# Kernel optimization log

Hardware: AMD Instinct MI355X
Metric: run time of the kernel (lower is better)

## Reference

```python
import jax, jax.numpy as jnp
import numpy as np

# Concrete segmented-polynomial instance (uniform 1d):
N = 8192      # nodes (rows of input 0 and of the indexed output)
E = 16384     # edges (batch dim of input 1 and of the per-edge product)
S = 16        # segments per operand (buffer_num_segments, same for all 3 operands)
EXT = 64      # operand_extent (uniform segment shape)
P = 2048      # num_paths of the single operation


def setup_inputs() -> dict:
    key = jax.random.key(0)
    k0, k1, k2, k3, k4, k5 = jax.random.split(key, 6)
    x = jax.random.normal(k0, (N, S * EXT), dtype=jnp.float32)          # node features
    y = jax.random.normal(k1, (E, S * EXT), dtype=jnp.float32)          # edge features
    idx_in = jax.random.randint(k2, (E,), 0, N, dtype=jnp.int32)        # gather index for input 0
    idx_out = jax.random.randint(k3, (E,), 0, N, dtype=jnp.int32)       # scatter index for output 0
    path_indices = jax.random.randint(k4, (P, 3), 0, S, dtype=jnp.int32)  # (i_x, j_y, k_out) per path
    path_coefficients = jax.random.normal(k5, (P,), dtype=jnp.float32)
    return {
        "x": x, "y": y,
        "idx_in": idx_in, "idx_out": idx_out,
        "path_indices": path_indices,
        "path_coefficients": path_coefficients,
    }


def reference(x, y, idx_in, idx_out, path_indices, path_coefficients):
    # Dense path-coefficient tensor C[k, i, j]: duplicate paths accumulate,
    # missing (k,i,j) triples are zero. This is the math-dtype (fp32) contraction
    # the uniform-1d kernel performs over segments of equal extent.
    C = jnp.zeros((S, S, S), dtype=x.dtype).at[
        path_indices[:, 2], path_indices[:, 0], path_indices[:, 1]
    ].add(path_coefficients)

    xr = x.reshape(N, S, EXT)[idx_in]   # gather (BATCH_DIM_INDEXED input): [E, S, EXT]
    yr = y.reshape(E, S, EXT)           # batched input:                    [E, S, EXT]

    # out_e[e, k, c] = sum_{i,j} C[k,i,j] * xr[e,i,c] * yr[e,j,c]
    out_e = jnp.einsum('kij,eic,ejc->ekc', C, xr, yr)

    # scatter-add (BATCH_DIM_INDEXED output) into N output rows
    out = jnp.zeros((N, S, EXT), dtype=x.dtype).at[idx_out].add(out_e)
    return out.reshape(N, S * EXT)
```

## Files before the change

### kernel.cpp

```cpp
#include <hip/hip_runtime.h>
#include <hip/hip_bf16.h>

#define N_NODES 8192
#define E_EDGES 16384
#define S_SEG   16
#define EXT     64
#define P_PATHS 2048
#define ROW     1024
#define L_SLOTS 8
#define NWAVES  (E_EDGES / L_SLOTS)
#define NBLK    (NWAVES / 4)

typedef _Float16 f16x8  __attribute__((ext_vector_type(8)));
typedef _Float16 f16x4  __attribute__((ext_vector_type(4)));
typedef _Float16 half2v __attribute__((ext_vector_type(2)));
typedef float    f32x4  __attribute__((ext_vector_type(4)));

#define WS_CMAT  0
#define WS_HIST  8192
#define WS_CURS  40960
#define WS_ROWS  73728
#define WS_ELIST 106512
#define WS_XRS   172048
#define WS_NDS   237584

__global__ void prep(const int* __restrict__ pidx, const float* __restrict__ pcoef,
                     _Float16* __restrict__ Cmat, int* __restrict__ hist) {
    const int tid = threadIdx.x;
    if (blockIdx.x < 32) { hist[blockIdx.x * 256 + tid] = 0; return; }
    __shared__ float sC[S_SEG * S_SEG * S_SEG];
    for (int i = tid; i < 4096; i += 256) sC[i] = 0.f;
    __syncthreads();
    for (int p = tid; p < P_PATHS; p += 256) {
        int i = pidx[3 * p + 0];
        int j = pidx[3 * p + 1];
        int k = pidx[3 * p + 2];
        atomicAdd(&sC[(k * S_SEG + i) * S_SEG + j], pcoef[p]);
    }
    __syncthreads();
    for (int i = tid; i < 4096; i += 256) Cmat[i] = (_Float16)sC[i];
}

__global__ void hist_k(const int* __restrict__ idx_out, int* __restrict__ hist) {
    const int e = blockIdx.x * 256 + threadIdx.x;
    atomicAdd(&hist[idx_out[e]], 1);
}

__global__ __launch_bounds__(256) void scan_k(const int* __restrict__ hist,
                                              int* __restrict__ rows,
                                              int* __restrict__ cursor) {
    __shared__ int part[256];
    const int t = threadIdx.x;
    const int base = t * 32;
    int loc[32];
    int s = 0;
#pragma unroll
    for (int i = 0; i < 32; ++i) { loc[i] = s; s += hist[base + i]; }
    part[t] = s;
    __syncthreads();
    for (int off = 1; off < 256; off <<= 1) {
        int v = part[t];
        int u = (t >= off) ? part[t - off] : 0;
        __syncthreads();
        part[t] = v + u;
        __syncthreads();
    }
    const int excl = (t == 0) ? 0 : part[t - 1];
#pragma unroll
    for (int i = 0; i < 32; ++i) {
        int v = excl + loc[i];
        rows[base + i] = v;
        cursor[base + i] = v;
    }
    if (t == 255) rows[N_NODES] = part[255];
}

__global__ void scatter_k(const int* __restrict__ idx_in, const int* __restrict__ idx_out,
                          int* __restrict__ cursor, int* __restrict__ elist,
                          int* __restrict__ xrs, int* __restrict__ nds) {
    const int e = blockIdx.x * 256 + threadIdx.x;
    const int nd = idx_out[e];
    const int pos = atomicAdd(&cursor[nd], 1);
    elist[pos] = e;
    xrs[pos]   = idx_in[e];
    nds[pos]   = nd;
}

__global__ __launch_bounds__(256) void zerofill_k(const int* __restrict__ rows,
                                                  float* __restrict__ out) {
    const int n = blockIdx.x * 4 + (threadIdx.x >> 6);
    const int lane = threadIdx.x & 63;
    const int beg = rows[n], end = rows[n + 1];
    const bool need = (beg == end) || ((beg / L_SLOTS) != ((end - 1) / L_SLOTS));
    if (!need) return;
    const float4 z = {0.f, 0.f, 0.f, 0.f};
    float* ob = out + (size_t)n * ROW + lane * 4;
#pragma unroll
    for (int r = 0; r < 4; ++r) *(float4*)(ob + r * 256) = z;
}

__global__ __launch_bounds__(256) void seg_poly_slots(
        const float* __restrict__ x, const float* __restrict__ y,
        const _Float16* __restrict__ Cmat,
        const int* __restrict__ elist, const int* __restrict__ xrs,
        const int* __restrict__ nds, float* __restrict__ out) {
    __shared__ __attribute__((aligned(16))) _Float16 sx_all[4][ROW];
    __shared__ __attribute__((aligned(16))) half2v   sy_all[4][512];

    const int tid  = threadIdx.x;
    const int lane = tid & 63;
    const int wv   = tid >> 6;
    _Float16* sxh = sx_all[wv];
    half2v*   syp = sy_all[wv];

    const int wid = blockIdx.x * 4 + wv;
    const int s0  = wid * L_SLOTS;

    const int quad = lane >> 4;
    const int m    = lane & 15;
    const int jb2  = (quad & 1) * 4;
    const int ih   = quad >> 1;
    const int jp   = lane >> 3;
    const int cq   = (lane & 7) * 8;

    int e_[L_SLOTS], xr_[L_SLOTS], nd_[L_SLOTS];
    {
        int4 a = *(const int4*)(elist + s0); int4 b = *(const int4*)(elist + s0 + 4);
        e_[0]=a.x; e_[1]=a.y; e_[2]=a.z; e_[3]=a.w; e_[4]=b.x; e_[5]=b.y; e_[6]=b.z; e_[7]=b.w;
        a = *(const int4*)(xrs + s0); b = *(const int4*)(xrs + s0 + 4);
        xr_[0]=a.x; xr_[1]=a.y; xr_[2]=a.z; xr_[3]=a.w; xr_[4]=b.x; xr_[5]=b.y; xr_[6]=b.z; xr_[7]=b.w;
        a = *(const int4*)(nds + s0); b = *(const int4*)(nds + s0 + 4);
        nd_[0]=a.x; nd_[1]=a.y; nd_[2]=a.z; nd_[3]=a.w; nd_[4]=b.x; nd_[5]=b.y; nd_[6]=b.z; nd_[7]=b.w;
    }
    const bool prev_same = (s0 > 0)                  && (nds[s0 - 1]       == nd_[0]);
    const bool next_same = (s0 + L_SLOTS < E_EDGES)  && (nds[s0 + L_SLOTS] == nd_[L_SLOTS - 1]);

    f16x8 afrag[8];
    {
        const _Float16* basep = Cmat + m * 256 + quad * 8;
#pragma unroll
        for (int kk = 0; kk < 8; ++kk) afrag[kk] = *(const f16x8*)(basep + kk * 32);
    }

    float4 xbuf[2][4], ybuf[2][4];
    auto issue = [&](int t, int b) {
        const float* xp = x + (size_t)xr_[t] * ROW;
        const float* yp = y + (size_t)e_[t] * ROW;
#pragma unroll
        for (int k4 = 0; k4 < 4; ++k4)
            xbuf[b][k4] = *(const float4*)(xp + k4 * 256 + lane * 4);
        ybuf[b][0] = *(const float4*)(yp + (2 * jp)     * EXT + cq);
        ybuf[b][1] = *(const float4*)(yp + (2 * jp)     * EXT + cq + 4);
        ybuf[b][2] = *(const float4*)(yp + (2 * jp + 1) * EXT + cq);
        ybuf[b][3] = *(const float4*)(yp + (2 * jp + 1) * EXT + cq + 4);
    };
    issue(0, 0);

    f32x4 acc[4];
#pragma unroll
    for (int ct = 0; ct < 4; ++ct) acc[ct] = f32x4{0.f, 0.f, 0.f, 0.f};
    int segStart = 0;

#pragma unroll
    for (int t = 0; t < L_SLOTS; ++t) {
        const int b = t & 1;
        if (t + 1 < L_SLOTS) issue(t + 1, b ^ 1);

#pragma unroll
        for (int k4 = 0; k4 < 4; ++k4) {
            const float4 v = xbuf[b][k4];
            *(f16x4*)(sxh + k4 * 256 + lane * 4) =
                f16x4{(_Float16)v.x, (_Float16)v.y, (_Float16)v.z, (_Float16)v.w};
        }
        {
            const float4 a0 = ybuf[b][0], a1 = ybuf[b][1];
            const float4 c0 = ybuf[b][2], c1 = ybuf[b][3];
            *(f16x8*)(syp + jp * 64 + cq) =
                f16x8{(_Float16)a0.x, (_Float16)c0.x, (_Float16)a0.y, (_Float16)c0.y,
                      (_Float16)a0.z, (_Float16)c0.z, (_Float16)a0.w, (_Float16)c0.w};
            *(f16x8*)(syp + jp * 64 + cq + 4) =
                f16x8{(_Float16)a1.x, (_Float16)c1.x, (_Float16)a1.y, (_Float16)c1.y,
                      (_Float16)a1.z, (_Float16)c1.z, (_Float16)a1.w, (_Float16)c1.w};
        }

#pragma unroll
        for (int ct = 0; ct < 4; ++ct) {
            const int c = ct * 16 + m;
            half2v ypk[4];
#pragma unroll
            for (int r = 0; r < 4; ++r) ypk[r] = syp[(jb2 + r) * 64 + c];
#pragma unroll
            for (int kk = 0; kk < 8; ++kk) {
                const _Float16 xh = sxh[(2 * kk + ih) * EXT + c];
                const half2v hx = {xh, xh};
                const half2v b0 = hx * ypk[0];
                const half2v b1 = hx * ypk[1];
                const half2v b2 = hx * ypk[2];
                const half2v b3 = hx * ypk[3];
                const f16x8 bfrag = {b0[0], b0[1], b1[0], b1[1],
                                     b2[0], b2[1], b3[0], b3[1]};
                acc[ct] = __builtin_amdgcn_mfma_f32_16x16x32_f16(
                              afrag[kk], bfrag, acc[ct], 0, 0, 0);
            }
        }

        const bool last = (t == L_SLOTS - 1);
        if (last || nd_[t + 1] != nd_[t]) {
            const bool shared = (segStart == 0 && prev_same) || (last && next_same);
            float* ob = out + (size_t)nd_[t] * ROW;
            if (shared) {
#pragma unroll
                for (int ct = 0; ct < 4; ++ct)
#pragma unroll
                    for (int r = 0; r < 4; ++r)
                        atomicAdd(ob + (quad * 4 + r) * EXT + ct * 16 + m, acc[ct][r]);
            } else {
#pragma unroll
                for (int ct = 0; ct < 4; ++ct)
#pragma unroll
                    for (int r = 0; r < 4; ++r)
                        ob[(quad * 4 + r) * EXT + ct * 16 + m] = acc[ct][r];
            }
#pragma unroll
            for (int ct = 0; ct < 4; ++ct) acc[ct] = f32x4{0.f, 0.f, 0.f, 0.f};
            segStart = t + 1;
        }
    }
}

extern "C" void kernel_launch(void* const* d_in, const int* in_sizes, int n_in,
                              void* d_out, int out_size, void* d_ws, size_t ws_size,
                              hipStream_t stream) {
    const float* x       = (const float*)d_in[0];
    const float* y       = (const float*)d_in[1];
    const int*   idx_in  = (const int*)d_in[2];
    const int*   idx_out = (const int*)d_in[3];
    const int*   pidx    = (const int*)d_in[4];
    const float* pcoef   = (const float*)d_in[5];
    float* out           = (float*)d_out;

    char* ws = (char*)d_ws;
    _Float16* Cmat = (_Float16*)(ws + WS_CMAT);
    int* hist      = (int*)(ws + WS_HIST);
    int* cursor    = (int*)(ws + WS_CURS);
    int* rows      = (int*)(ws + WS_ROWS);
    int* elist     = (int*)(ws + WS_ELIST);
    int* xrs       = (int*)(ws + WS_XRS);
    int* nds       = (int*)(ws + WS_NDS);

    prep<<<33, 256, 0, stream>>>(pidx, pcoef, Cmat, hist);
    hist_k<<<E_EDGES / 256, 256, 0, stream>>>(idx_out, hist);
    scan_k<<<1, 256, 0, stream>>>(hist, rows, cursor);
    scatter_k<<<E_EDGES / 256, 256, 0, stream>>>(idx_in, idx_out, cursor, elist, xrs, nds);
    zerofill_k<<<N_NODES / 4, 256, 0, stream>>>(rows, out);
    seg_poly_slots<<<NBLK, 256, 0, stream>>>(x, y, Cmat, elist, xrs, nds, out);
}
```

Baseline: 161.5 us.

## Split each edge group across two waves by channel half and merge scatter/zero kernels

Each group of 8 sorted edges is now handled by two waves, each covering 32 of the 64 channels. This doubles the wave count and halves per-wave registers and LDS, raising occupancy and parallelism. Loads are prefetched two slots ahead, and launch_bounds requests 4 blocks per CU. The scatter and zero-fill kernels are fused into one launch to save a kernel launch. The trade-off is that each wave redundantly loads the C-matrix fragments and the edge index lists.

After: 159.7 us. No clear change (-1.2%).

```diff
diff --git a/kernel.cpp b/kernel.cpp
--- a/kernel.cpp
+++ b/kernel.cpp
@@ -8,7 +8,8 @@
 #define P_PATHS 2048
 #define ROW     1024
 #define L_SLOTS 8
-#define NWAVES  (E_EDGES / L_SLOTS)
+#define NGROUPS (E_EDGES / L_SLOTS)
+#define NWAVES  (NGROUPS * 2)
 #define NBLK    (NWAVES / 4)
 
 typedef _Float16 f16x8  __attribute__((ext_vector_type(8)));
@@ -75,37 +76,39 @@
     if (t == 255) rows[N_NODES] = part[255];
 }
 
-__global__ void scatter_k(const int* __restrict__ idx_in, const int* __restrict__ idx_out,
-                          int* __restrict__ cursor, int* __restrict__ elist,
-                          int* __restrict__ xrs, int* __restrict__ nds) {
-    const int e = blockIdx.x * 256 + threadIdx.x;
-    const int nd = idx_out[e];
-    const int pos = atomicAdd(&cursor[nd], 1);
-    elist[pos] = e;
-    xrs[pos]   = idx_in[e];
-    nds[pos]   = nd;
-}
-
-__global__ __launch_bounds__(256) void zerofill_k(const int* __restrict__ rows,
-                                                  float* __restrict__ out) {
-    const int n = blockIdx.x * 4 + (threadIdx.x >> 6);
-    const int lane = threadIdx.x & 63;
-    const int beg = rows[n], end = rows[n + 1];
-    const bool need = (beg == end) || ((beg / L_SLOTS) != ((end - 1) / L_SLOTS));
-    if (!need) return;
-    const float4 z = {0.f, 0.f, 0.f, 0.f};
-    float* ob = out + (size_t)n * ROW + lane * 4;
-#pragma unroll
-    for (int r = 0; r < 4; ++r) *(float4*)(ob + r * 256) = z;
-}
-
-__global__ __launch_bounds__(256) void seg_poly_slots(
+__global__ __launch_bounds__(256) void scatter_zero_k(
+        const int* __restrict__ idx_in, const int* __restrict__ idx_out,
+        int* __restrict__ cursor, int* __restrict__ elist,
+        int* __restrict__ xrs, int* __restrict__ nds,
+        const int* __restrict__ rows, float* __restrict__ out) {
+    const int b = blockIdx.x;
+    if (b < E_EDGES / 256) {
+        const int e = b * 256 + threadIdx.x;
+        const int nd = idx_out[e];
+        const int pos = atomicAdd(&cursor[nd], 1);
+        elist[pos] = e;
+        xrs[pos]   = idx_in[e];
+        nds[pos]   = nd;
+    } else {
+        const int n = (b - E_EDGES / 256) * 4 + (threadIdx.x >> 6);
+        const int lane = threadIdx.x & 63;
+        const int beg = rows[n], end = rows[n + 1];
+        const bool need = (beg == end) || ((beg / L_SLOTS) != ((end - 1) / L_SLOTS));
+        if (!need) return;
+        const float4 z = {0.f, 0.f, 0.f, 0.f};
+        float* ob = out + (size_t)n * ROW + lane * 4;
+#pragma unroll
+        for (int r = 0; r < 4; ++r) *(float4*)(ob + r * 256) = z;
+    }
+}
+
+__global__ __launch_bounds__(256, 4) void seg_poly_slots(
         const float* __restrict__ x, const float* __restrict__ y,
         const _Float16* __restrict__ Cmat,
         const int* __restrict__ elist, const int* __restrict__ xrs,
         const int* __restrict__ nds, float* __restrict__ out) {
-    __shared__ __attribute__((aligned(16))) _Float16 sx_all[4][ROW];
-    __shared__ __attribute__((aligned(16))) half2v   sy_all[4][512];
+    __shared__ __attribute__((aligned(16))) _Float16 sx_all[4][S_SEG * 32];
+    __shared__ __attribute__((aligned(16))) half2v   sy_all[4][8 * 32];
 
     const int tid  = threadIdx.x;
     const int lane = tid & 63;
@@ -114,14 +117,17 @@
     half2v*   syp = sy_all[wv];
 
     const int wid = blockIdx.x * 4 + wv;
-    const int s0  = wid * L_SLOTS;
+    const int g   = wid >> 1;
+    const int h   = wid & 1;
+    const int s0  = g * L_SLOTS;
+    const int c0  = h * 32;
 
     const int quad = lane >> 4;
     const int m    = lane & 15;
     const int jb2  = (quad & 1) * 4;
     const int ih   = quad >> 1;
     const int jp   = lane >> 3;
-    const int cq   = (lane & 7) * 8;
+    const int c4   = (lane & 7) * 4;
 
     int e_[L_SLOTS], xr_[L_SLOTS], nd_[L_SLOTS];
     {
@@ -142,56 +148,49 @@
         for (int kk = 0; kk < 8; ++kk) afrag[kk] = *(const f16x8*)(basep + kk * 32);
     }
 
-    float4 xbuf[2][4], ybuf[2][4];
+    float4 xbuf[2][2], ybuf[2][2];
     auto issue = [&](int t, int b) {
-        const float* xp = x + (size_t)xr_[t] * ROW;
-        const float* yp = y + (size_t)e_[t] * ROW;
-#pragma unroll
-        for (int k4 = 0; k4 < 4; ++k4)
-            xbuf[b][k4] = *(const float4*)(xp + k4 * 256 + lane * 4);
-        ybuf[b][0] = *(const float4*)(yp + (2 * jp)     * EXT + cq);
-        ybuf[b][1] = *(const float4*)(yp + (2 * jp)     * EXT + cq + 4);
-        ybuf[b][2] = *(const float4*)(yp + (2 * jp + 1) * EXT + cq);
-        ybuf[b][3] = *(const float4*)(yp + (2 * jp + 1) * EXT + cq + 4);
+        const float* xp = x + (size_t)xr_[t] * ROW + c0;
+        const float* yp = y + (size_t)e_[t] * ROW + c0;
+        xbuf[b][0] = *(const float4*)(xp + jp * EXT + c4);
+        xbuf[b][1] = *(const float4*)(xp + (jp + 8) * EXT + c4);
+        ybuf[b][0] = *(const float4*)(yp + (2 * jp)     * EXT + c4);
+        ybuf[b][1] = *(const float4*)(yp + (2 * jp + 1) * EXT + c4);
     };
     issue(0, 0);
-
-    f32x4 acc[4];
-#pragma unroll
-    for (int ct = 0; ct < 4; ++ct) acc[ct] = f32x4{0.f, 0.f, 0.f, 0.f};
+    issue(1, 1);
+
+    f32x4 acc[2];
+#pragma unroll
+    for (int ct = 0; ct < 2; ++ct) acc[ct] = f32x4{0.f, 0.f, 0.f, 0.f};
     int segStart = 0;
 
 #pragma unroll
     for (int t = 0; t < L_SLOTS; ++t) {
         const int b = t & 1;
-        if (t + 1 < L_SLOTS) issue(t + 1, b ^ 1);
-
-#pragma unroll
-        for (int k4 = 0; k4 < 4; ++k4) {
-            const float4 v = xbuf[b][k4];
-            *(f16x4*)(sxh + k4 * 256 + lane * 4) =
-                f16x4{(_Float16)v.x, (_Float16)v.y, (_Float16)v.z, (_Float16)v.w};
+
+        {
+            const float4 v0 = xbuf[b][0], v1 = xbuf[b][1];
+            *(f16x4*)(sxh + jp * 32 + c4) =
+                f16x4{(_Float16)v0.x, (_Float16)v0.y, (_Float16)v0.z, (_Float16)v0.w};
+            *(f16x4*)(sxh + (jp + 8) * 32 + c4) =
+                f16x4{(_Float16)v1.x, (_Float16)v1.y, (_Float16)v1.z, (_Float16)v1.w};
+            const float4 a0 = ybuf[b][0], a1 = ybuf[b][1];
+            *(f16x8*)(syp + jp * 32 + c4) =
+                f16x8{(_Float16)a0.x, (_Float16)a1.x, (_Float16)a0.y, (_Float16)a1.y,
+                      (_Float16)a0.z, (_Float16)a1.z, (_Float16)a0.w, (_Float16)a1.w};
         }
-        {
-            const float4 a0 = ybuf[b][0], a1 = ybuf[b][1];
-            const float4 c0 = ybuf[b][2], c1 = ybuf[b][3];
-            *(f16x8*)(syp + jp * 64 + cq) =
-                f16x8{(_Float16)a0.x, (_Float16)c0.x, (_Float16)a0.y, (_Float16)c0.y,
-                      (_Float16)a0.z, (_Float16)c0.z, (_Float16)a0.w, (_Float16)c0.w};
-            *(f16x8*)(syp + jp * 64 + cq + 4) =
-                f16x8{(_Float16)a1.x, (_Float16)c1.x, (_Float16)a1.y, (_Float16)c1.y,
-                      (_Float16)a1.z, (_Float16)c1.z, (_Float16)a1.w, (_Float16)c1.w};
-        }
-
-#pragma unroll
-        for (int ct = 0; ct < 4; ++ct) {
-            const int c = ct * 16 + m;
+        if (t + 2 < L_SLOTS) issue(t + 2, b);
+
+#pragma unroll
+        for (int ct = 0; ct < 2; ++ct) {
+            const int cl = ct * 16 + m;
             half2v ypk[4];
 #pragma unroll
-            for (int r = 0; r < 4; ++r) ypk[r] = syp[(jb2 + r) * 64 + c];
+            for (int r = 0; r < 4; ++r) ypk[r] = syp[(jb2 + r) * 32 + cl];
 #pragma unroll
             for (int kk = 0; kk < 8; ++kk) {
-                const _Float16 xh = sxh[(2 * kk + ih) * EXT + c];
+                const _Float16 xh = sxh[(2 * kk + ih) * 32 + cl];
                 const half2v hx = {xh, xh};
                 const half2v b0 = hx * ypk[0];
                 const half2v b1 = hx * ypk[1];
@@ -207,22 +206,22 @@
         const bool last = (t == L_SLOTS - 1);
         if (last || nd_[t + 1] != nd_[t]) {
             const bool shared = (segStart == 0 && prev_same) || (last && next_same);
-            float* ob = out + (size_t)nd_[t] * ROW;
+            float* ob = out + (size_t)nd_[t] * ROW + c0;
             if (shared) {
 #pragma unroll
-                for (int ct = 0; ct < 4; ++ct)
+                for (int ct = 0; ct < 2; ++ct)
 #pragma unroll
                     for (int r = 0; r < 4; ++r)
                         atomicAdd(ob + (quad * 4 + r) * EXT + ct * 16 + m, acc[ct][r]);
             } else {
 #pragma unroll
-                for (int ct = 0; ct < 4; ++ct)
+                for (int ct = 0; ct < 2; ++ct)
 #pragma unroll
                     for (int r = 0; r < 4; ++r)
                         ob[(quad * 4 + r) * EXT + ct * 16 + m] = acc[ct][r];
             }
 #pragma unroll
-            for (int ct = 0; ct < 4; ++ct) acc[ct] = f32x4{0.f, 0.f, 0.f, 0.f};
+            for (int ct = 0; ct < 2; ++ct) acc[ct] = f32x4{0.f, 0.f, 0.f, 0.f};
             segStart = t + 1;
         }
     }
@@ -251,7 +250,7 @@
     prep<<<33, 256, 0, stream>>>(pidx, pcoef, Cmat, hist);
     hist_k<<<E_EDGES / 256, 256, 0, stream>>>(idx_out, hist);
     scan_k<<<1, 256, 0, stream>>>(hist, rows, cursor);
-    scatter_k<<<E_EDGES / 256, 256, 0, stream>>>(idx_in, idx_out, cursor, elist, xrs, nds);
-    zerofill_k<<<N_NODES / 4, 256, 0, stream>>>(rows, out);
+    scatter_zero_k<<<E_EDGES / 256 + N_NODES / 4, 256, 0, stream>>>(
+        idx_in, idx_out, cursor, elist, xrs, nds, rows, out);
     seg_poly_slots<<<NBLK, 256, 0, stream>>>(x, y, Cmat, elist, xrs, nds, out);
 }
```

## Replace sort-by-destination pipeline with per-edge atomic scatter kernel

Applied to the files above, without the earlier changes.

Drops the histogram, scan and counting-sort kernels that grouped edges by output node, and instead processes one edge per wave, atomically adding its 16x64 result into the output row. Zeroing the output is merged into the coefficient-prep kernel, so the launch count falls from six to two. The cost is an atomic add for every output element of every edge (about 16M fp32 atomics) instead of mostly plain stores. The per-edge kernel also loses the double-buffered prefetch across edges and reloads the C fragments for each edge.

Measured after the change: 178.0 us. +10.2%, slower.

```diff
diff --git a/kernel.cpp b/kernel.cpp
--- a/kernel.cpp
+++ b/kernel.cpp
@@ -1,5 +1,4 @@
 #include <hip/hip_runtime.h>
-#include <hip/hip_bf16.h>
 
 #define N_NODES 8192
 #define E_EDGES 16384
@@ -7,9 +6,6 @@
 #define EXT     64
 #define P_PATHS 2048
 #define ROW     1024
-#define L_SLOTS 8
-#define NWAVES  (E_EDGES / L_SLOTS)
-#define NBLK    (NWAVES / 4)
 
 typedef _Float16 f16x8  __attribute__((ext_vector_type(8)));
 typedef _Float16 f16x4  __attribute__((ext_vector_type(4)));
@@ -17,93 +13,36 @@
 typedef float    f32x4  __attribute__((ext_vector_type(4)));
 
 #define WS_CMAT  0
-#define WS_HIST  8192
-#define WS_CURS  40960
-#define WS_ROWS  73728
-#define WS_ELIST 106512
-#define WS_XRS   172048
-#define WS_NDS   237584
 
-__global__ void prep(const int* __restrict__ pidx, const float* __restrict__ pcoef,
-                     _Float16* __restrict__ Cmat, int* __restrict__ hist) {
+__global__ __launch_bounds__(256) void prep_zero(
+        const int* __restrict__ pidx, const float* __restrict__ pcoef,
+        _Float16* __restrict__ Cmat, float* __restrict__ out) {
     const int tid = threadIdx.x;
-    if (blockIdx.x < 32) { hist[blockIdx.x * 256 + tid] = 0; return; }
-    __shared__ float sC[S_SEG * S_SEG * S_SEG];
-    for (int i = tid; i < 4096; i += 256) sC[i] = 0.f;
-    __syncthreads();
-    for (int p = tid; p < P_PATHS; p += 256) {
-        int i = pidx[3 * p + 0];
-        int j = pidx[3 * p + 1];
-        int k = pidx[3 * p + 2];
-        atomicAdd(&sC[(k * S_SEG + i) * S_SEG + j], pcoef[p]);
+    if (blockIdx.x == 0) {
+        __shared__ float sC[S_SEG * S_SEG * S_SEG];
+        for (int i = tid; i < 4096; i += 256) sC[i] = 0.f;
+        __syncthreads();
+        for (int p = tid; p < P_PATHS; p += 256) {
+            const int i = pidx[3 * p + 0];
+            const int j = pidx[3 * p + 1];
+            const int k = pidx[3 * p + 2];
+            atomicAdd(&sC[(k * S_SEG + i) * S_SEG + j], pcoef[p]);
+        }
+        __syncthreads();
+        for (int i = tid; i < 4096; i += 256) Cmat[i] = (_Float16)sC[i];
+    } else {
+        const float4 z = {0.f, 0.f, 0.f, 0.f};
+        float* ob = out + (size_t)(blockIdx.x - 1) * 4096 + tid * 4;
+#pragma unroll
+        for (int r = 0; r < 4; ++r) *(float4*)(ob + r * 1024) = z;
     }
-    __syncthreads();
-    for (int i = tid; i < 4096; i += 256) Cmat[i] = (_Float16)sC[i];
 }
 
-__global__ void hist_k(const int* __restrict__ idx_out, int* __restrict__ hist) {
-    const int e = blockIdx.x * 256 + threadIdx.x;
-    atomicAdd(&hist[idx_out[e]], 1);
-}
-
-__global__ __launch_bounds__(256) void scan_k(const int* __restrict__ hist,
-                                              int* __restrict__ rows,
-                                              int* __restrict__ cursor) {
-    __shared__ int part[256];
-    const int t = threadIdx.x;
-    const int base = t * 32;
-    int loc[32];
-    int s = 0;
-#pragma unroll
-    for (int i = 0; i < 32; ++i) { loc[i] = s; s += hist[base + i]; }
-    part[t] = s;
-    __syncthreads();
-    for (int off = 1; off < 256; off <<= 1) {
-        int v = part[t];
-        int u = (t >= off) ? part[t - off] : 0;
-        __syncthreads();
-        part[t] = v + u;
-        __syncthreads();
-    }
-    const int excl = (t == 0) ? 0 : part[t - 1];
-#pragma unroll
-    for (int i = 0; i < 32; ++i) {
-        int v = excl + loc[i];
-        rows[base + i] = v;
-        cursor[base + i] = v;
-    }
-    if (t == 255) rows[N_NODES] = part[255];
-}
-
-__global__ void scatter_k(const int* __restrict__ idx_in, const int* __restrict__ idx_out,
-                          int* __restrict__ cursor, int* __restrict__ elist,
-                          int* __restrict__ xrs, int* __restrict__ nds) {
-    const int e = blockIdx.x * 256 + threadIdx.x;
-    const int nd = idx_out[e];
-    const int pos = atomicAdd(&cursor[nd], 1);
-    elist[pos] = e;
-    xrs[pos]   = idx_in[e];
-    nds[pos]   = nd;
-}
-
-__global__ __launch_bounds__(256) void zerofill_k(const int* __restrict__ rows,
-                                                  float* __restrict__ out) {
-    const int n = blockIdx.x * 4 + (threadIdx.x >> 6);
-    const int lane = threadIdx.x & 63;
-    const int beg = rows[n], end = rows[n + 1];
-    const bool need = (beg == end) || ((beg / L_SLOTS) != ((end - 1) / L_SLOTS));
-    if (!need) return;
-    const float4 z = {0.f, 0.f, 0.f, 0.f};
-    float* ob = out + (size_t)n * ROW + lane * 4;
-#pragma unroll
-    for (int r = 0; r < 4; ++r) *(float4*)(ob + r * 256) = z;
-}
-
-__global__ __launch_bounds__(256) void seg_poly_slots(
+__global__ __launch_bounds__(256) void edge_atomic(
         const float* __restrict__ x, const float* __restrict__ y,
         const _Float16* __restrict__ Cmat,
-        const int* __restrict__ elist, const int* __restrict__ xrs,
-        const int* __restrict__ nds, float* __restrict__ out) {
+        const int* __restrict__ idx_in, const int* __restrict__ idx_out,
+        float* __restrict__ out) {
     __shared__ __attribute__((aligned(16))) _Float16 sx_all[4][ROW];
     __shared__ __attribute__((aligned(16))) half2v   sy_all[4][512];
 
@@ -113,8 +52,9 @@
     _Float16* sxh = sx_all[wv];
     half2v*   syp = sy_all[wv];
 
-    const int wid = blockIdx.x * 4 + wv;
-    const int s0  = wid * L_SLOTS;
+    const int e  = blockIdx.x * 4 + wv;
+    const int xr = idx_in[e];
+    const int nd = idx_out[e];
 
     const int quad = lane >> 4;
     const int m    = lane & 15;
@@ -123,18 +63,6 @@
     const int jp   = lane >> 3;
     const int cq   = (lane & 7) * 8;
 
-    int e_[L_SLOTS], xr_[L_SLOTS], nd_[L_SLOTS];
-    {
-        int4 a = *(const int4*)(elist + s0); int4 b = *(const int4*)(elist + s0 + 4);
-        e_[0]=a.x; e_[1]=a.y; e_[2]=a.z; e_[3]=a.w; e_[4]=b.x; e_[5]=b.y; e_[6]=b.z; e_[7]=b.w;
-        a = *(const int4*)(xrs + s0); b = *(const int4*)(xrs + s0 + 4);
-        xr_[0]=a.x; xr_[1]=a.y; xr_[2]=a.z; xr_[3]=a.w; xr_[4]=b.x; xr_[5]=b.y; xr_[6]=b.z; xr_[7]=b.w;
-        a = *(const int4*)(nds + s0); b = *(const int4*)(nds + s0 + 4);
-        nd_[0]=a.x; nd_[1]=a.y; nd_[2]=a.z; nd_[3]=a.w; nd_[4]=b.x; nd_[5]=b.y; nd_[6]=b.z; nd_[7]=b.w;
-    }
-    const bool prev_same = (s0 > 0)                  && (nds[s0 - 1]       == nd_[0]);
-    const bool next_same = (s0 + L_SLOTS < E_EDGES)  && (nds[s0 + L_SLOTS] == nd_[L_SLOTS - 1]);
-
     f16x8 afrag[8];
     {
         const _Float16* basep = Cmat + m * 256 + quad * 8;
@@ -142,90 +70,65 @@
         for (int kk = 0; kk < 8; ++kk) afrag[kk] = *(const f16x8*)(basep + kk * 32);
     }
 
-    float4 xbuf[2][4], ybuf[2][4];
-    auto issue = [&](int t, int b) {
-        const float* xp = x + (size_t)xr_[t] * ROW;
-        const float* yp = y + (size_t)e_[t] * ROW;
+    const float* xp = x + (size_t)xr * ROW;
+    const float* yp = y + (size_t)e  * ROW;
+    float4 xb[4], yb[4];
 #pragma unroll
-        for (int k4 = 0; k4 < 4; ++k4)
-            xbuf[b][k4] = *(const float4*)(xp + k4 * 256 + lane * 4);
-        ybuf[b][0] = *(const float4*)(yp + (2 * jp)     * EXT + cq);
-        ybuf[b][1] = *(const float4*)(yp + (2 * jp)     * EXT + cq + 4);
-        ybuf[b][2] = *(const float4*)(yp + (2 * jp + 1) * EXT + cq);
-        ybuf[b][3] = *(const float4*)(yp + (2 * jp + 1) * EXT + cq + 4);
-    };
-    issue(0, 0);
+    for (int k4 = 0; k4 < 4; ++k4)
+        xb[k4] = *(const float4*)(xp + k4 * 256 + lane * 4);
+    yb[0] = *(const float4*)(yp + (2 * jp)     * EXT + cq);
+    yb[1] = *(const float4*)(yp + (2 * jp)     * EXT + cq + 4);
+    yb[2] = *(const float4*)(yp + (2 * jp + 1) * EXT + cq);
+    yb[3] = *(const float4*)(yp + (2 * jp + 1) * EXT + cq + 4);
+
+#pragma unroll
+    for (int k4 = 0; k4 < 4; ++k4) {
+        const float4 v = xb[k4];
+        *(f16x4*)(sxh + k4 * 256 + lane * 4) =
+            f16x4{(_Float16)v.x, (_Float16)v.y, (_Float16)v.z, (_Float16)v.w};
+    }
+    {
+        const float4 a0 = yb[0], a1 = yb[1];
+        const float4 c0 = yb[2], c1 = yb[3];
+        *(f16x8*)(syp + jp * 64 + cq) =
+            f16x8{(_Float16)a0.x, (_Float16)c0.x, (_Float16)a0.y, (_Float16)c0.y,
+                  (_Float16)a0.z, (_Float16)c0.z, (_Float16)a0.w, (_Float16)c0.w};
+        *(f16x8*)(syp + jp * 64 + cq + 4) =
+            f16x8{(_Float16)a1.x, (_Float16)c1.x, (_Float16)a1.y, (_Float16)c1.y,
+                  (_Float16)a1.z, (_Float16)c1.z, (_Float16)a1.w, (_Float16)c1.w};
+    }
 
     f32x4 acc[4];
 #pragma unroll
     for (int ct = 0; ct < 4; ++ct) acc[ct] = f32x4{0.f, 0.f, 0.f, 0.f};
-    int segStart = 0;
 
 #pragma unroll
-    for (int t = 0; t < L_SLOTS; ++t) {
-        const int b = t & 1;
-        if (t + 1 < L_SLOTS) issue(t + 1, b ^ 1);
-
+    for (int ct = 0; ct < 4; ++ct) {
+        const int c = ct * 16 + m;
+        half2v ypk[4];
 #pragma unroll
-        for (int k4 = 0; k4 < 4; ++k4) {
-            const float4 v = xbuf[b][k4];
-            *(f16x4*)(sxh + k4 * 256 + lane * 4) =
-                f16x4{(_Float16)v.x, (_Float16)v.y, (_Float16)v.z, (_Float16)v.w};
-        }
-        {
-            const float4 a0 = ybuf[b][0], a1 = ybuf[b][1];
-            const float4 c0 = ybuf[b][2], c1 = ybuf[b][3];
-            *(f16x8*)(syp + jp * 64 + cq) =
-                f16x8{(_Float16)a0.x, (_Float16)c0.x, (_Float16)a0.y, (_Float16)c0.y,
-                      (_Float16)a0.z, (_Float16)c0.z, (_Float16)a0.w, (_Float16)c0.w};
-            *(f16x8*)(syp + jp * 64 + cq + 4) =
-                f16x8{(_Float16)a1.x, (_Float16)c1.x, (_Float16)a1.y, (_Float16)c1.y,
-                      (_Float16)a1.z, (_Float16)c1.z, (_Float16)a1.w, (_Float16)c1.w};
-        }
-
+        for (int r = 0; r < 4; ++r) ypk[r] = syp[(jb2 + r) * 64 + c];
 #pragma unroll
-        for (int ct = 0; ct < 4; ++ct) {
-            const int c = ct * 16 + m;
-            half2v ypk[4];
-#pragma unroll
-            for (int r = 0; r < 4; ++r) ypk[r] = syp[(jb2 + r) * 64 + c];
-#pragma unroll
-            for (int kk = 0; kk < 8; ++kk) {
-                const _Float16 xh = sxh[(2 * kk + ih) * EXT + c];
-                const half2v hx = {xh, xh};
-                const half2v b0 = hx * ypk[0];
-                const half2v b1 = hx * ypk[1];
-                const half2v b2 = hx * ypk[2];
-                const half2v b3 = hx * ypk[3];
-                const f16x8 bfrag = {b0[0], b0[1], b1[0], b1[1],
-                                     b2[0], b2[1], b3[0], b3[1]};
-                acc[ct] = __builtin_amdgcn_mfma_f32_16x16x32_f16(
-                              afrag[kk], bfrag, acc[ct], 0, 0, 0);
-            }
-        }
-
-        const bool last = (t == L_SLOTS - 1);
-        if (last || nd_[t + 1] != nd_[t]) {
-            const bool shared = (segStart == 0 && prev_same) || (last && next_same);
-            float* ob = out + (size_t)nd_[t] * ROW;
-            if (shared) {
-#pragma unroll
-                for (int ct = 0; ct < 4; ++ct)
-#pragma unroll
-                    for (int r = 0; r < 4; ++r)
-                        atomicAdd(ob + (quad * 4 + r) * EXT + ct * 16 + m, acc[ct][r]);
-            } else {
-#pragma unroll
-                for (int ct = 0; ct < 4; ++ct)
-#pragma unroll
-                    for (int r = 0; r < 4; ++r)
-                        ob[(quad * 4 + r) * EXT + ct * 16 + m] = acc[ct][r];
-            }
-#pragma unroll
-            for (int ct = 0; ct < 4; ++ct) acc[ct] = f32x4{0.f, 0.f, 0.f, 0.f};
-            segStart = t + 1;
+        for (int kk = 0; kk < 8; ++kk) {
+            const _Float16 xh = sxh[(2 * kk + ih) * EXT + c];
+            const half2v hx = {xh, xh};
+            const half2v b0 = hx * ypk[0];
+            const half2v b1 = hx * ypk[1];
+            const half2v b2 = hx * ypk[2];
+            const half2v b3 = hx * ypk[3];
+            const f16x8 bfrag = {b0[0], b0[1], b1[0], b1[1],
+                                 b2[0], b2[1], b3[0], b3[1]};
+            acc[ct] = __builtin_amdgcn_mfma_f32_16x16x32_f16(
+                          afrag[kk], bfrag, acc[ct], 0, 0, 0);
         }
     }
+
+    float* ob = out + (size_t)nd * ROW;
+#pragma unroll
+    for (int ct = 0; ct < 4; ++ct)
+#pragma unroll
+        for (int r = 0; r < 4; ++r)
+            atomicAdd(ob + (quad * 4 + r) * EXT + ct * 16 + m, acc[ct][r]);
 }
 
 extern "C" void kernel_launch(void* const* d_in, const int* in_sizes, int n_in,
@@ -239,19 +142,8 @@
     const float* pcoef   = (const float*)d_in[5];
     float* out           = (float*)d_out;
 
-    char* ws = (char*)d_ws;
-    _Float16* Cmat = (_Float16*)(ws + WS_CMAT);
-    int* hist      = (int*)(ws + WS_HIST);
-    int* cursor    = (int*)(ws + WS_CURS);
-    int* rows      = (int*)(ws + WS_ROWS);
-    int* elist     = (int*)(ws + WS_ELIST);
-    int* xrs       = (int*)(ws + WS_XRS);
-    int* nds       = (int*)(ws + WS_NDS);
+    _Float16* Cmat = (_Float16*)((char*)d_ws + WS_CMAT);
 
-    prep<<<33, 256, 0, stream>>>(pidx, pcoef, Cmat, hist);
-    hist_k<<<E_EDGES / 256, 256, 0, stream>>>(idx_out, hist);
-    scan_k<<<1, 256, 0, stream>>>(hist, rows, cursor);
-    scatter_k<<<E_EDGES / 256, 256, 0, stream>>>(idx_in, idx_out, cursor, elist, xrs, nds);
-    zerofill_k<<<N_NODES / 4, 256, 0, stream>>>(rows, out);
-    seg_poly_slots<<<NBLK, 256, 0, stream>>>(x, y, Cmat, elist, xrs, nds, out);
+    prep_zero<<<1 + N_NODES * ROW / 4096, 256, 0, stream>>>(pidx, pcoef, Cmat, out);
+    edge_atomic<<<E_EDGES / 4, 256, 0, stream>>>(x, y, Cmat, idx_in, idx_out, out);
 }
```
